# Kernel tuning notes

Hardware: AMD Instinct MI355X
Metric: run time of the kernel (lower is better)

The kernel has to match this reference:

```python
import jax, jax.numpy as jnp
import numpy as np

B, H, W, C = 16, 64, 64, 256
WS = 8          # window_size
SHIFT = 4       # shift_size
HEADS = 8
HEAD_DIM = C // HEADS
N = WS * WS     # tokens per window
HID = 4 * C     # mlp hidden
EPS = 1e-5


def _rel_pos_index():
    coords = np.stack(np.meshgrid(np.arange(WS), np.arange(WS), indexing='ij'))  # [2,WS,WS]
    flat = coords.reshape(2, -1)                                                  # [2,N]
    rel = (flat[:, :, None] - flat[:, None, :]).transpose(1, 2, 0)                # [N,N,2]
    rel[:, :, 0] += WS - 1
    rel[:, :, 1] += WS - 1
    rel[:, :, 0] *= 2 * WS - 1
    return rel.sum(-1).astype(np.int32)                                           # [N,N]


def _attn_mask():
    # shifted-window region ids, identical to get_img_mask (shift == WS//2)
    img = np.zeros((H, W), dtype=np.float32)
    cnt = 0
    for hs in (slice(0, H - WS), slice(H - WS, H - SHIFT), slice(H - SHIFT, H)):
        for ws_ in (slice(0, W - WS), slice(W - WS, W - SHIFT), slice(W - SHIFT, W)):
            img[hs, ws_] = cnt
            cnt += 1
    mw = img.reshape(H // WS, WS, W // WS, WS).transpose(0, 2, 1, 3).reshape(-1, N)  # [nW,N]
    diff = mw[:, None, :] - mw[:, :, None]
    return np.where(diff != 0, -100.0, 0.0).astype(np.float32)                        # [nW,N,N]


def window_partition(x):
    # [B,H,W,C] -> [B*nW, N, C]
    x = x.reshape(B, H // WS, WS, W // WS, WS, C)
    return x.transpose(0, 1, 3, 2, 4, 5).reshape(-1, N, C)


def window_reverse(w):
    # [B*nW, WS, WS, C] -> [B,H,W,C]
    x = w.reshape(B, H // WS, W // WS, WS, WS, C)
    return x.transpose(0, 1, 3, 2, 4, 5).reshape(B, H, W, C)


def layernorm(x, g, b):
    mu = jnp.mean(x, -1, keepdims=True)
    var = jnp.mean(jnp.square(x - mu), -1, keepdims=True)
    return (x - mu) * jax.lax.rsqrt(var + EPS) * g + b


def setup_inputs() -> dict:
    key = jax.random.key(0)
    ks = jax.random.split(key, 12)
    s = 0.02
    return {
        'x': jax.random.normal(ks[0], (B, H, W, C), jnp.float32),
        'ln1_g': jnp.ones((C,), jnp.float32),
        'ln1_b': jnp.zeros((C,), jnp.float32),
        'qkv_w': jax.random.normal(ks[1], (C, 3 * C), jnp.float32) * s,
        'qkv_b': jnp.zeros((3 * C,), jnp.float32),
        'proj_w': jax.random.normal(ks[2], (C, C), jnp.float32) * s,
        'proj_b': jnp.zeros((C,), jnp.float32),
        'rel_bias_table': jax.random.normal(ks[3], ((2 * WS - 1) ** 2, HEADS), jnp.float32) * s,
        'ln2_g': jnp.ones((C,), jnp.float32),
        'ln2_b': jnp.zeros((C,), jnp.float32),
        'mlp_w1': jax.random.normal(ks[4], (C, HID), jnp.float32) * s,
        'mlp_b1': jnp.zeros((HID,), jnp.float32),
        'mlp_w2': jax.random.normal(ks[5], (HID, C), jnp.float32) * s,
        'mlp_b2': jnp.zeros((C,), jnp.float32),
        'rel_index': jnp.asarray(_rel_pos_index()),  # [N,N] int32, constant
    }


def reference(x, ln1_g, ln1_b, qkv_w, qkv_b, proj_w, proj_b, rel_bias_table,
              ln2_g, ln2_b, mlp_w1, mlp_b1, mlp_w2, mlp_b2, rel_index):
    attn_mask = jnp.asarray(_attn_mask())                 # [nW,N,N]
    nW = attn_mask.shape[0]

    shortcut = x.reshape(B, H * W, C)
    h = layernorm(shortcut, ln1_g, ln1_b).reshape(B, H, W, C)

    # cyclic shift + window partition
    h = jnp.roll(h, shift=(-SHIFT, -SHIFT), axis=(1, 2))
    xw = window_partition(h)                              # [B*nW, N, C]

    # window attention with relative position bias
    qkv = xw @ qkv_w + qkv_b                              # [B*nW, N, 3C]
    qkv = qkv.reshape(-1, N, 3, HEADS, HEAD_DIM).transpose(2, 0, 3, 1, 4)
    q, k, v = qkv[0], qkv[1], qkv[2]                      # [B*nW, heads, N, hd]
    attn = jnp.einsum('whnd,whmd->whnm', q * (HEAD_DIM ** -0.5), k)
    bias = rel_bias_table[rel_index]                      # [N,N,heads]
    attn = attn + bias.transpose(2, 0, 1)[None]           # [B*nW,heads,N,N]
    attn = attn.reshape(B, nW, HEADS, N, N) + attn_mask[None, :, None]
    attn = jax.nn.softmax(attn.reshape(-1, HEADS, N, N), axis=-1)
    out = jnp.einsum('whnm,whmd->whnd', attn, v)
    out = out.transpose(0, 2, 1, 3).reshape(-1, N, C)
    out = out @ proj_w + proj_b                           # [B*nW, N, C]

    # window reverse + reverse shift
    out = window_reverse(out.reshape(-1, WS, WS, C))
    out = jnp.roll(out, shift=(SHIFT, SHIFT), axis=(1, 2)).reshape(B, H * W, C)

    h = shortcut + out
    m = layernorm(h, ln2_g, ln2_b)
    m = jax.nn.gelu(m @ mlp_w1 + mlp_b1) @ mlp_w2 + mlp_b2
    h = h + m
    return h.reshape(B, H, W, C)
```

## Files before the change

### kernel.cpp

```cpp
#include <hip/hip_runtime.h>


typedef __attribute__((ext_vector_type(8))) short bf16x8;
typedef __attribute__((ext_vector_type(4))) float f32x4;
typedef __attribute__((ext_vector_type(16))) float f32x16;

__device__ __forceinline__ float bf2f(unsigned short h) {
    union { unsigned int u; float f; } c; c.u = ((unsigned int)h) << 16; return c.f;
}
__device__ __forceinline__ unsigned short f2bf(float f) {
    union { float f; unsigned int u; } c; c.f = f;
    unsigned int u = c.u;
    return (unsigned short)((u + 0x7FFFu + ((u >> 16) & 1u)) >> 16);
}
__device__ __forceinline__ unsigned int cvtpk_bf16(float lo, float hi) {
    unsigned int r;
    asm volatile("v_cvt_pk_bf16_f32 %0, %1, %2" : "=v"(r) : "v"(lo), "v"(hi));
    return r;
}
__device__ __forceinline__ void perm32swap(unsigned int& a, unsigned int& b) {
    asm volatile("v_permlane32_swap_b32 %0, %1" : "+v"(a), "+v"(b));
}
__device__ __forceinline__ int remap_row(int row) {
    int b  = row >> 12;
    int w6 = (row >> 6) & 63;
    int n  = row & 63;
    int hp = (((w6 >> 3) << 3) + (n >> 3) + 4) & 63;
    int wp = (((w6 & 7) << 3) + (n & 7) + 4) & 63;
    return (b << 12) | (hp << 6) | wp;
}
__device__ __forceinline__ float gelu_f(float v) {
    float u = 1.5957691216057308f * (v + 0.044715f * v * v * v);
    return v / (1.0f + __expf(-u));
}
__device__ __forceinline__ void gload16(const unsigned short* g, unsigned short* l) {
    __builtin_amdgcn_global_load_lds(
        (const __attribute__((address_space(1))) void*)g,
        (__attribute__((address_space(3))) void*)l, 16, 0, 0);
}

__global__ __launch_bounds__(256) void ln_kernel(
    const float* __restrict__ in, const float* __restrict__ g,
    const float* __restrict__ b, unsigned short* __restrict__ out, int remap)
{
    int wave = threadIdx.x >> 6, lane = threadIdx.x & 63;
    int row = (blockIdx.x << 2) + wave;
    int src = remap ? remap_row(row) : row;
    float4 xv = *(const float4*)(in + (size_t)src * 256 + (lane << 2));
    float s  = xv.x + xv.y + xv.z + xv.w;
    float ss = xv.x*xv.x + xv.y*xv.y + xv.z*xv.z + xv.w*xv.w;
#pragma unroll
    for (int off = 32; off; off >>= 1) {
        s  += __shfl_xor(s,  off, 64);
        ss += __shfl_xor(ss, off, 64);
    }
    float mu  = s * (1.0f / 256.0f);
    float inv = rsqrtf(ss * (1.0f / 256.0f) - mu * mu + 1e-5f);
    float4 gv = *(const float4*)(g + (lane << 2));
    float4 bv = *(const float4*)(b + (lane << 2));
    ushort4 o;
    o.x = f2bf((xv.x - mu) * inv * gv.x + bv.x);
    o.y = f2bf((xv.y - mu) * inv * gv.y + bv.y);
    o.z = f2bf((xv.z - mu) * inv * gv.z + bv.z);
    o.w = f2bf((xv.w - mu) * inv * gv.w + bv.w);
    *(ushort4*)(out + (size_t)row * 256 + (lane << 2)) = o;
}

__device__ __forceinline__ void convT_body(
    const float* __restrict__ in, unsigned short* __restrict__ out,
    int K, int N, int b, float (*t)[33], int tid)
{
    int kb = K >> 5;
    int bk = (b % kb) << 5;
    int bn = (b / kb) << 5;
    int r = tid >> 5, c = tid & 31;
#pragma unroll
    for (int i = 0; i < 4; ++i)
        t[r + i * 8][c] = in[(size_t)(bk + r + i * 8) * N + bn + c];
    __syncthreads();
#pragma unroll
    for (int i = 0; i < 4; ++i)
        out[(size_t)(bn + r + i * 8) * K + bk + c] = f2bf(t[c][r + i * 8]);
}

__global__ __launch_bounds__(256) void prep_kernel(
    const float* __restrict__ qkv_w, const float* __restrict__ proj_w,
    const float* __restrict__ w1, const float* __restrict__ w2,
    unsigned short* __restrict__ qkvT, unsigned short* __restrict__ prjT,
    unsigned short* __restrict__ w1T, unsigned short* __restrict__ w2T,
    const float* __restrict__ table, const int* __restrict__ relidx,
    float* __restrict__ bexp)
{
    __shared__ float t[32][33];
    const int b = blockIdx.x, tid = threadIdx.x;
    if      (b < 192) convT_body(qkv_w, qkvT, 256,  768, b,       t, tid);
    else if (b < 256) convT_body(proj_w, prjT, 256,  256, b - 192, t, tid);
    else if (b < 512) convT_body(w1,    w1T,  256, 1024, b - 256, t, tid);
    else if (b < 768) convT_body(w2,    w2T, 1024,  256, b - 512, t, tid);
    else {
        int i = (b - 768) * 256 + tid;
        int head = i >> 12;
        int q = (i >> 6) & 63;
        int k = i & 63;
        bexp[i] = table[relidx[q * 64 + k] * 8 + head];
    }
}

template<int OUT_BF16, int DO_GELU, int RESID, int QSCALE>
__global__ __launch_bounds__(256) void mgemm_kernel(
    const unsigned short* __restrict__ A, const unsigned short* __restrict__ BT,
    const float* __restrict__ bias, void* __restrict__ outp,
    const float* __restrict__ resid, int M, int N, int K)
{
    __shared__ unsigned short As[2][128 * 32];
    __shared__ unsigned short Bs[2][128 * 32];

    const int cpx = (int)gridDim.x >> 3;
    const int bid = ((int)blockIdx.x & 7) * cpx + ((int)blockIdx.x >> 3);

    const int nb = N >> 7;
    const int m0 = (bid / nb) << 7;
    const int n0 = (bid % nb) << 7;
    const int tid  = threadIdx.x;
    const int wid  = tid >> 6;
    const int lane = tid & 63;
    const int wm = (wid >> 1) << 6;
    const int wn = (wid & 1) << 6;

    const unsigned short* Ag = A  + (size_t)m0 * K;
    const unsigned short* Bg = BT + (size_t)n0 * K;
    const int s0 = tid, s1 = tid + 256;
    const size_t ra0 = (size_t)(s0 >> 2) * K + (((s0 & 3) ^ ((s0 >> 2) & 3)) << 3);
    const size_t ra1 = (size_t)(s1 >> 2) * K + (((s1 & 3) ^ ((s1 >> 2) & 3)) << 3);

    f32x4 acc[4][4] = {};
    const int fr = lane & 15;
    const int fq = lane >> 4;
    const int axor = ((fq ^ (fr & 3)) << 3);

    gload16(Ag + ra0, As[0] + s0 * 8);
    gload16(Ag + ra1, As[0] + s1 * 8);
    gload16(Bg + ra0, Bs[0] + s0 * 8);
    gload16(Bg + ra1, Bs[0] + s1 * 8);
    __syncthreads();

    int cur = 0;
    for (int k0 = 0; k0 < K; k0 += 32) {
        if (k0 + 32 < K) {
            const int nxt = cur ^ 1;
            gload16(Ag + ra0 + k0 + 32, As[nxt] + s0 * 8);
            gload16(Ag + ra1 + k0 + 32, As[nxt] + s1 * 8);
            gload16(Bg + ra0 + k0 + 32, Bs[nxt] + s0 * 8);
            gload16(Bg + ra1 + k0 + 32, Bs[nxt] + s1 * 8);
        }

        bf16x8 af[4], bfr[4];
#pragma unroll
        for (int i = 0; i < 4; ++i)
            af[i] = *(const bf16x8*)(As[cur] + (wm + i * 16 + fr) * 32 + axor);
#pragma unroll
        for (int j = 0; j < 4; ++j)
            bfr[j] = *(const bf16x8*)(Bs[cur] + (wn + j * 16 + fr) * 32 + axor);
#pragma unroll
        for (int j = 0; j < 4; ++j)
#pragma unroll
            for (int i = 0; i < 4; ++i)
                acc[j][i] = __builtin_amdgcn_mfma_f32_16x16x32_bf16(
                    bfr[j], af[i], acc[j][i], 0, 0, 0);
        __syncthreads();
        cur ^= 1;
    }

#pragma unroll
    for (int j = 0; j < 4; ++j) {
        const int colbase = n0 + wn + j * 16 + (fq << 2);
        const float4 b4 = *(const float4*)(bias + colbase);
#pragma unroll
        for (int i = 0; i < 4; ++i) {
            const int row = m0 + wm + i * 16 + fr;
            float v0 = acc[j][i][0] + b4.x;
            float v1 = acc[j][i][1] + b4.y;
            float v2 = acc[j][i][2] + b4.z;
            float v3 = acc[j][i][3] + b4.w;
            if (QSCALE && colbase < 256) {
                v0 *= 0.17677669529663687f; v1 *= 0.17677669529663687f;
                v2 *= 0.17677669529663687f; v3 *= 0.17677669529663687f;
            }
            if (DO_GELU) {
                v0 = gelu_f(v0); v1 = gelu_f(v1); v2 = gelu_f(v2); v3 = gelu_f(v3);
            }
            if (OUT_BF16) {
                uint2 pp;
                pp.x = cvtpk_bf16(v0, v1);
                pp.y = cvtpk_bf16(v2, v3);
                *(uint2*)((unsigned short*)outp + (size_t)row * N + colbase) = pp;
            } else {
                const int orow = (RESID == 2) ? remap_row(row) : row;
                float4 o4;
                if (RESID) {
                    const float4 r4 = *(const float4*)(resid + (size_t)orow * N + colbase);
                    o4.x = v0 + r4.x; o4.y = v1 + r4.y;
                    o4.z = v2 + r4.z; o4.w = v3 + r4.w;
                } else {
                    o4.x = v0; o4.y = v1; o4.z = v2; o4.w = v3;
                }
                *(float4*)((float*)outp + (size_t)orow * N + colbase) = o4;
            }
        }
    }
}

__global__ __launch_bounds__(64, 3) void attn_kernel(
    const unsigned short* __restrict__ qkv,
    const float* __restrict__ bexp,
    unsigned short* __restrict__ out)
{
    __shared__ unsigned short VT[2048];
    const int bid  = blockIdx.x;
    const int widx = bid & 1023;
    const int head = bid >> 10;
    const int l  = threadIdx.x;
    const int lo = l & 31, hi = l >> 5;

    const unsigned short* base = qkv + (size_t)widx * 64 * 768;

#pragma unroll
    for (int c = 0; c < 4; ++c) {
        union { bf16x8 v; unsigned short s[8]; } u;
        u.v = *(const bf16x8*)(base + (size_t)l * 768 + 512 + head * 32 + c * 8);
#pragma unroll
        for (int e = 0; e < 8; ++e) {
            int d = c * 8 + e;
            int wb = ((d * 64 + l) * 2) ^ ((d & 7) << 4);
            *(unsigned short*)((char*)VT + wb) = u.s[e];
        }
    }

    f32x16 acc[2][2] = {};
#pragma unroll
    for (int kd = 0; kd < 2; ++kd) {
        const int coff = head * 32 + kd * 16 + hi * 8;
        bf16x8 kf0 = *(const bf16x8*)(base + (size_t)lo        * 768 + 256 + coff);
        bf16x8 kf1 = *(const bf16x8*)(base + (size_t)(32 + lo) * 768 + 256 + coff);
        bf16x8 qf0 = *(const bf16x8*)(base + (size_t)lo        * 768 + coff);
        bf16x8 qf1 = *(const bf16x8*)(base + (size_t)(32 + lo) * 768 + coff);
        acc[0][0] = __builtin_amdgcn_mfma_f32_32x32x16_bf16(kf0, qf0, acc[0][0], 0, 0, 0);
        acc[0][1] = __builtin_amdgcn_mfma_f32_32x32x16_bf16(kf0, qf1, acc[0][1], 0, 0, 0);
        acc[1][0] = __builtin_amdgcn_mfma_f32_32x32x16_bf16(kf1, qf0, acc[1][0], 0, 0, 0);
        acc[1][1] = __builtin_amdgcn_mfma_f32_32x32x16_bf16(kf1, qf1, acc[1][1], 0, 0, 0);
    }

#pragma unroll
    for (int qb = 0; qb < 2; ++qb) {
        const float* bq = bexp + head * 4096 + (qb * 32 + lo) * 64;
#pragma unroll
        for (int kb = 0; kb < 2; ++kb)
#pragma unroll
            for (int j = 0; j < 4; ++j) {
                float4 b4 = *(const float4*)(bq + kb * 32 + j * 8 + hi * 4);
                acc[kb][qb][4 * j + 0] += b4.x;
                acc[kb][qb][4 * j + 1] += b4.y;
                acc[kb][qb][4 * j + 2] += b4.z;
                acc[kb][qb][4 * j + 3] += b4.w;
            }
    }

    const int w6 = widx & 63;
    if (((w6 >> 3) == 7) || ((w6 & 7) == 7)) {
#pragma unroll
        for (int qb = 0; qb < 2; ++qb) {
            int nq = qb * 32 + lo;
            int phq = ((w6 >> 3) << 3) + (nq >> 3), pwq = ((w6 & 7) << 3) + (nq & 7);
            int rq = ((phq < 56) ? 0 : ((phq < 60) ? 1 : 2)) * 3
                   + ((pwq < 56) ? 0 : ((pwq < 60) ? 1 : 2));
#pragma unroll
            for (int kb = 0; kb < 2; ++kb)
#pragma unroll
                for (int r = 0; r < 16; ++r) {
                    int nk = kb * 32 + (r & 3) + 8 * (r >> 2) + 4 * hi;
                    int phk = ((w6 >> 3) << 3) + (nk >> 3), pwk = ((w6 & 7) << 3) + (nk & 7);
                    int rk = ((phk < 56) ? 0 : ((phk < 60) ? 1 : 2)) * 3
                           + ((pwk < 56) ? 0 : ((pwk < 60) ? 1 : 2));
                    if (rk != rq) acc[kb][qb][r] -= 100.0f;
                }
        }
    }

#pragma unroll
    for (int qb = 0; qb < 2; ++qb) {
        float mx = acc[0][qb][0];
#pragma unroll
        for (int r = 1; r < 16; ++r) mx = fmaxf(mx, acc[0][qb][r]);
#pragma unroll
        for (int r = 0; r < 16; ++r) mx = fmaxf(mx, acc[1][qb][r]);
        mx = fmaxf(mx, __shfl_xor(mx, 32, 64));
        float sum = 0.f;
#pragma unroll
        for (int kb = 0; kb < 2; ++kb)
#pragma unroll
            for (int r = 0; r < 16; ++r) {
                float e = __expf(acc[kb][qb][r] - mx);
                acc[kb][qb][r] = e;
                sum += e;
            }
        sum += __shfl_xor(sum, 32, 64);
        float inv = 1.0f / sum;
#pragma unroll
        for (int kb = 0; kb < 2; ++kb)
#pragma unroll
            for (int r = 0; r < 16; ++r) acc[kb][qb][r] *= inv;
    }

    f32x16 o[2] = {};
#pragma unroll
    for (int ks = 0; ks < 4; ++ks) {
        const int s8 = (ks & 1) * 8, kb = ks >> 1;
        const int rb = ((lo * 64 + 16 * ks + 8 * hi) * 2) ^ ((lo & 7) << 4);
        bf16x8 vb = *(const bf16x8*)((const char*)VT + rb);
#pragma unroll
        for (int qb = 0; qb < 2; ++qb) {
            unsigned int a0 = cvtpk_bf16(acc[kb][qb][s8 + 0], acc[kb][qb][s8 + 1]);
            unsigned int b0 = cvtpk_bf16(acc[kb][qb][s8 + 4], acc[kb][qb][s8 + 5]);
            unsigned int a1 = cvtpk_bf16(acc[kb][qb][s8 + 2], acc[kb][qb][s8 + 3]);
            unsigned int b1 = cvtpk_bf16(acc[kb][qb][s8 + 6], acc[kb][qb][s8 + 7]);
            perm32swap(a0, b0);
            perm32swap(a1, b1);
            union { unsigned int u[4]; bf16x8 v; } w;
            w.u[0] = a0; w.u[1] = a1; w.u[2] = b0; w.u[3] = b1;
            o[qb] = __builtin_amdgcn_mfma_f32_32x32x16_bf16(w.v, vb, o[qb], 0, 0, 0);
        }
    }

    unsigned short* ob = out + (size_t)widx * 64 * 256 + head * 32 + lo;
#pragma unroll
    for (int qb = 0; qb < 2; ++qb)
#pragma unroll
        for (int r = 0; r < 16; ++r) {
            int q = qb * 32 + (r & 3) + 8 * (r >> 2) + 4 * hi;
            ob[(size_t)q * 256] = f2bf(o[qb][r]);
        }
}

extern "C" void kernel_launch(void* const* d_in, const int* in_sizes, int n_in,
                              void* d_out, int out_size, void* d_ws, size_t ws_size,
                              hipStream_t stream)
{
    const float* x      = (const float*)d_in[0];
    const float* ln1_g  = (const float*)d_in[1];
    const float* ln1_b  = (const float*)d_in[2];
    const float* qkv_w  = (const float*)d_in[3];
    const float* qkv_b  = (const float*)d_in[4];
    const float* proj_w = (const float*)d_in[5];
    const float* proj_b = (const float*)d_in[6];
    const float* table  = (const float*)d_in[7];
    const float* ln2_g  = (const float*)d_in[8];
    const float* ln2_b  = (const float*)d_in[9];
    const float* w1     = (const float*)d_in[10];
    const float* b1     = (const float*)d_in[11];
    const float* w2     = (const float*)d_in[12];
    const float* b2     = (const float*)d_in[13];
    const int*   relidx = (const int*)d_in[14];
    float* out = (float*)d_out;

    char* w = (char*)d_ws;
    unsigned short* xw   = (unsigned short*)w;
    unsigned short* qkvb = (unsigned short*)(w + (32u << 20));
    float*          h2   = (float*)(w + (160u << 20));
    float*          bexp = (float*)(w + (224u << 20));
    unsigned short* qkvT = (unsigned short*)(w + (224u << 20) + (128u << 10));
    unsigned short* prjT = qkvT + 768 * 256;
    unsigned short* w1T  = prjT + 256 * 256;
    unsigned short* w2T  = w1T + 1024 * 256;

    prep_kernel<<<896, 256, 0, stream>>>(qkv_w, proj_w, w1, w2,
                                         qkvT, prjT, w1T, w2T,
                                         table, relidx, bexp);
    ln_kernel<<<16384, 256, 0, stream>>>(x, ln1_g, ln1_b, xw, 1);
    mgemm_kernel<1, 0, 0, 1><<<512 * 6, 256, 0, stream>>>(xw, qkvT, qkv_b, (void*)qkvb,
                                                          nullptr, 65536, 768, 256);
    attn_kernel<<<8192, 64, 0, stream>>>(qkvb, bexp, xw);
    mgemm_kernel<0, 0, 2, 0><<<512 * 2, 256, 0, stream>>>(xw, prjT, proj_b, (void*)h2,
                                                          x, 65536, 256, 256);
    ln_kernel<<<16384, 256, 0, stream>>>(h2, ln2_g, ln2_b, xw, 0);
    mgemm_kernel<1, 1, 0, 0><<<512 * 8, 256, 0, stream>>>(xw, w1T, b1, (void*)qkvb,
                                                          nullptr, 65536, 1024, 256);
    mgemm_kernel<0, 0, 1, 0><<<512 * 2, 256, 0, stream>>>(qkvb, w2T, b2, (void*)out,
                                                          h2, 65536, 256, 1024);
}
```

Baseline: 331.4 us.

## Replace LDS-staged GEMM with direct global-to-register fragment loads

The GEMM kernel drops its double-buffered shared-memory staging (global_load_lds plus __syncthreads) and has each wave load its MFMA A/B fragments straight from global memory into registers. It works in 128-wide K chunks and software-pipelines the A loads across the four sub-steps. The aim is to remove LDS traffic and block-wide barriers. In exchange, each wave re-reads its operands from global/L2 with no sharing across waves, and register pressure rises, which is relevant under the launch bound of 2.

```diff
diff --git a/kernel.cpp b/kernel.cpp
--- a/kernel.cpp
+++ b/kernel.cpp
@@ -32,11 +32,6 @@
 __device__ __forceinline__ float gelu_f(float v) {
     float u = 1.5957691216057308f * (v + 0.044715f * v * v * v);
     return v / (1.0f + __expf(-u));
-}
-__device__ __forceinline__ void gload16(const unsigned short* g, unsigned short* l) {
-    __builtin_amdgcn_global_load_lds(
-        (const __attribute__((address_space(1))) void*)g,
-        (__attribute__((address_space(3))) void*)l, 16, 0, 0);
 }
 
 __global__ __launch_bounds__(256) void ln_kernel(
@@ -107,14 +102,11 @@
 }
 
 template<int OUT_BF16, int DO_GELU, int RESID, int QSCALE>
-__global__ __launch_bounds__(256) void mgemm_kernel(
+__global__ __launch_bounds__(256, 2) void rgemm_kernel(
     const unsigned short* __restrict__ A, const unsigned short* __restrict__ BT,
     const float* __restrict__ bias, void* __restrict__ outp,
     const float* __restrict__ resid, int M, int N, int K)
 {
-    __shared__ unsigned short As[2][128 * 32];
-    __shared__ unsigned short Bs[2][128 * 32];
-
     const int cpx = (int)gridDim.x >> 3;
     const int bid = ((int)blockIdx.x & 7) * cpx + ((int)blockIdx.x >> 3);
 
@@ -126,50 +118,46 @@
     const int lane = tid & 63;
     const int wm = (wid >> 1) << 6;
     const int wn = (wid & 1) << 6;
-
-    const unsigned short* Ag = A  + (size_t)m0 * K;
-    const unsigned short* Bg = BT + (size_t)n0 * K;
-    const int s0 = tid, s1 = tid + 256;
-    const size_t ra0 = (size_t)(s0 >> 2) * K + (((s0 & 3) ^ ((s0 >> 2) & 3)) << 3);
-    const size_t ra1 = (size_t)(s1 >> 2) * K + (((s1 & 3) ^ ((s1 >> 2) & 3)) << 3);
-
-    f32x4 acc[4][4] = {};
     const int fr = lane & 15;
     const int fq = lane >> 4;
-    const int axor = ((fq ^ (fr & 3)) << 3);
-
-    gload16(Ag + ra0, As[0] + s0 * 8);
-    gload16(Ag + ra1, As[0] + s1 * 8);
-    gload16(Bg + ra0, Bs[0] + s0 * 8);
-    gload16(Bg + ra1, Bs[0] + s1 * 8);
-    __syncthreads();
-
-    int cur = 0;
-    for (int k0 = 0; k0 < K; k0 += 32) {
-        if (k0 + 32 < K) {
-            const int nxt = cur ^ 1;
-            gload16(Ag + ra0 + k0 + 32, As[nxt] + s0 * 8);
-            gload16(Ag + ra1 + k0 + 32, As[nxt] + s1 * 8);
-            gload16(Bg + ra0 + k0 + 32, Bs[nxt] + s0 * 8);
-            gload16(Bg + ra1 + k0 + 32, Bs[nxt] + s1 * 8);
-        }
-
-        bf16x8 af[4], bfr[4];
-#pragma unroll
-        for (int i = 0; i < 4; ++i)
-            af[i] = *(const bf16x8*)(As[cur] + (wm + i * 16 + fr) * 32 + axor);
+
+    const unsigned short* Ab = A  + (size_t)(m0 + wm + fr) * K + fq * 8;
+    const unsigned short* Bb = BT + (size_t)(n0 + wn + fr) * K + fq * 8;
+
+    f32x4 acc[4][4] = {};
+
+#define LOADA(dst, kk)                                                        \
+    {                                                                         \
+        _Pragma("unroll")                                                     \
+        for (int i_ = 0; i_ < 4; ++i_)                                        \
+            dst[i_] = *(const bf16x8*)(Ab + (size_t)i_ * 16 * K + (kk));      \
+    }
+
+    for (int kc = 0; kc < K; kc += 128) {
+        bf16x8 afA[4], afB[4];
+        LOADA(afA, kc);
+        bf16x8 bf[4][4];
 #pragma unroll
         for (int j = 0; j < 4; ++j)
-            bfr[j] = *(const bf16x8*)(Bs[cur] + (wn + j * 16 + fr) * 32 + axor);
-#pragma unroll
-        for (int j = 0; j < 4; ++j)
-#pragma unroll
-            for (int i = 0; i < 4; ++i)
-                acc[j][i] = __builtin_amdgcn_mfma_f32_16x16x32_bf16(
-                    bfr[j], af[i], acc[j][i], 0, 0, 0);
-        __syncthreads();
-        cur ^= 1;
-    }
+#pragma unroll
+            for (int t = 0; t < 4; ++t)
+                bf[j][t] = *(const bf16x8*)(Bb + (size_t)j * 16 * K + kc + t * 32);
+
+#pragma unroll
+        for (int t = 0; t < 4; ++t) {
+            if (t < 3) {
+                if (t & 1) LOADA(afA, kc + (t + 1) * 32)
+                else       LOADA(afB, kc + (t + 1) * 32)
+            }
+#pragma unroll
+            for (int j = 0; j < 4; ++j)
+#pragma unroll
+                for (int i = 0; i < 4; ++i)
+                    acc[j][i] = __builtin_amdgcn_mfma_f32_16x16x32_bf16(
+                        bf[j][t], (t & 1) ? afB[i] : afA[i], acc[j][i], 0, 0, 0);
+        }
+    }
+#undef LOADA
 
 #pragma unroll
     for (int j = 0; j < 4; ++j) {
@@ -376,14 +364,14 @@
                                          qkvT, prjT, w1T, w2T,
                                          table, relidx, bexp);
     ln_kernel<<<16384, 256, 0, stream>>>(x, ln1_g, ln1_b, xw, 1);
-    mgemm_kernel<1, 0, 0, 1><<<512 * 6, 256, 0, stream>>>(xw, qkvT, qkv_b, (void*)qkvb,
+    rgemm_kernel<1, 0, 0, 1><<<512 * 6, 256, 0, stream>>>(xw, qkvT, qkv_b, (void*)qkvb,
                                                           nullptr, 65536, 768, 256);
     attn_kernel<<<8192, 64, 0, stream>>>(qkvb, bexp, xw);
-    mgemm_kernel<0, 0, 2, 0><<<512 * 2, 256, 0, stream>>>(xw, prjT, proj_b, (void*)h2,
+    rgemm_kernel<0, 0, 2, 0><<<512 * 2, 256, 0, stream>>>(xw, prjT, proj_b, (void*)h2,
                                                           x, 65536, 256, 256);
     ln_kernel<<<16384, 256, 0, stream>>>(h2, ln2_g, ln2_b, xw, 0);
-    mgemm_kernel<1, 1, 0, 0><<<512 * 8, 256, 0, stream>>>(xw, w1T, b1, (void*)qkvb,
+    rgemm_kernel<1, 1, 0, 0><<<512 * 8, 256, 0, stream>>>(xw, w1T, b1, (void*)qkvb,
                                                           nullptr, 65536, 1024, 256);
-    mgemm_kernel<0, 0, 1, 0><<<512 * 2, 256, 0, stream>>>(qkvb, w2T, b2, (void*)out,
+    rgemm_kernel<0, 0, 1, 0><<<512 * 2, 256, 0, stream>>>(qkvb, w2T, b2, (void*)out,
                                                           h2, 65536, 256, 1024);
 }
```

New measurement: 550.2 us. 1.66x slower.
